# Optimization experiments

Hardware: AMD Instinct MI355X
Metric: run time of the kernel (lower is better)

Reference implementation:

```python
import jax, jax.numpy as jnp
import numpy as np

N, E, G = 10000, 40000, 128          # nodes, edges, graphs
NF, EF, H, NH, GD, L = 92, 50, 64, 10, 108, 5  # feat dims, hidden, heads, global dim, layers
EPS = 1e-5

def _lrelu(v):
    return jax.nn.leaky_relu(v, 0.2)

def setup_inputs() -> dict:
    key = jax.random.key(0)
    ks = jax.random.split(key, 24)
    def rn(k, shp, s=0.05):
        return jax.random.normal(k, shp, jnp.float32) * s
    return {
        "x": jax.random.normal(ks[0], (N, NF), jnp.float32),
        "edge_index": jax.random.randint(ks[1], (2, E), 0, N, dtype=jnp.int32),
        "edge_attr": jax.random.normal(ks[2], (E, EF), jnp.float32),
        "batch_idx": jnp.sort(jax.random.randint(ks[3], (N,), 0, G, dtype=jnp.int32)),
        "global_features": jax.random.normal(ks[4], (G, GD), jnp.float32),
        "node_W": rn(ks[5], (NF, H)), "node_b": jnp.zeros((H,), jnp.float32),
        "edge_W": rn(ks[6], (EF, H)), "edge_b": jnp.zeros((H,), jnp.float32),
        "conv_W": rn(ks[7], (L, 2 * H, NH * H)),
        "conv_att": rn(ks[8], (L, NH, 2 * H)),
        "conv_b": jnp.zeros((L, H), jnp.float32),
        "conv_gamma": jnp.ones((L, NH), jnp.float32),
        "conv_beta": jnp.zeros((L, NH), jnp.float32),
        "ga_W1": rn(ks[9], (H + GD, H)), "ga_b1": jnp.zeros((H,), jnp.float32),
        "ga_W2": rn(ks[10], (H, 1)), "ga_b2": jnp.zeros((1,), jnp.float32),
        "out_W1": rn(ks[11], (H, H)), "out_b1": jnp.zeros((H,), jnp.float32),
        "out_W2": rn(ks[12], (H, 1)), "out_b2": jnp.zeros((1,), jnp.float32),
    }

def reference(x, edge_index, edge_attr, batch_idx, global_features,
              node_W, node_b, edge_W, edge_b,
              conv_W, conv_att, conv_b, conv_gamma, conv_beta,
              ga_W1, ga_b1, ga_W2, ga_b2, out_W1, out_b1, out_W2, out_b2):
    row, col = edge_index[0], edge_index[1]
    # embeddings
    h = _lrelu(x @ node_W + node_b)            # [N, H]
    ea = _lrelu(edge_attr @ edge_W + edge_b)   # [E, H]
    initial = h
    inv_std = 1.0 / jnp.sqrt(1.0 + EPS)        # DiffGroupNorm eval: running mean=0, var=1
    for i in range(L):
        xi = jnp.concatenate([h[row], ea], axis=-1)               # [E, 2H]
        xj = jnp.concatenate([h[col], ea], axis=-1)
        hi = _lrelu(xi @ conv_W[i]).reshape(E, NH, H)             # [E, NH, H]
        hj = _lrelu(xj @ conv_W[i]).reshape(E, NH, H)
        alpha = jnp.sum(jnp.concatenate([hi, hj], -1) * conv_att[i][None], -1)  # [E, NH]
        alpha = _lrelu(alpha)
        alpha = alpha * inv_std * conv_gamma[i] + conv_beta[i]
        alpha = jax.nn.softmax(alpha, axis=1)                     # softmax over heads
        msg = (hj * alpha[..., None]).reshape(E, NH * H)
        agg = jax.ops.segment_sum(msg, row, num_segments=N).reshape(N, NH, H)
        h_new = agg.mean(axis=1) + conv_b[i]
        h = h + h_new if i > 0 else h_new
    h = h + initial
    # global attention: softmax over nodes within each graph
    g = global_features[batch_idx]                                 # [N, GD]
    s = _lrelu(jnp.concatenate([h, g], -1) @ ga_W1 + ga_b1)
    score = (s @ ga_W2 + ga_b2)[:, 0]                              # [N]
    smax = jax.ops.segment_max(score, batch_idx, num_segments=G)
    ex = jnp.exp(score - smax[batch_idx])
    denom = jax.ops.segment_sum(ex, batch_idx, num_segments=G)
    w = (ex / denom[batch_idx])[:, None]
    h = h * w
    pooled = jax.ops.segment_sum(h, batch_idx, num_segments=G)     # [G, H]
    out = jax.nn.relu(pooled @ out_W1 + out_b1) @ out_W2 + out_b2
    return out[:, 0]
```

## Files before the change

### kernel.cpp

```cpp
#include <hip/hip_runtime.h>

#define LRELU(v) ((v) > 0.f ? (v) : 0.2f * (v))

template <int CTRL, int RMASK>
__device__ __forceinline__ float dpp_add(float v) {
  int moved = __builtin_amdgcn_update_dpp(0, __builtin_bit_cast(int, v), CTRL,
                                          RMASK, 0xf, true);
  return v + __builtin_bit_cast(float, moved);
}
__device__ __forceinline__ float wave_sum(float v) {
  v = dpp_add<0x111, 0xf>(v);
  v = dpp_add<0x112, 0xf>(v);
  v = dpp_add<0x114, 0xf>(v);
  v = dpp_add<0x118, 0xf>(v);
  v = dpp_add<0x142, 0xa>(v);
  v = dpp_add<0x143, 0xc>(v);
  return __builtin_bit_cast(
      float, __builtin_amdgcn_readlane(__builtin_bit_cast(int, v), 63));
}

__global__ __launch_bounds__(256) void embed2_kernel(
    const float* __restrict__ x, const float* __restrict__ nW,
    const float* __restrict__ nb, float* __restrict__ h0, int N_,
    const float* __restrict__ eattr, const float* __restrict__ eW,
    const float* __restrict__ eb, float* __restrict__ ea, int E_,
    int nodeBlocks) {
  const int lane = threadIdx.x & 63;
  const float *X, *W, *b;
  float* out;
  int M, K, r;
  if ((int)blockIdx.x < nodeBlocks) {
    r = blockIdx.x * 4 + (threadIdx.x >> 6);
    X = x; W = nW; b = nb; out = h0; M = N_; K = 92;
  } else {
    r = (blockIdx.x - nodeBlocks) * 4 + (threadIdx.x >> 6);
    X = eattr; W = eW; b = eb; out = ea; M = E_; K = 50;
  }
  r = __builtin_amdgcn_readfirstlane(r);
  if (r >= M) return;
  float acc = b[lane];
  const float* Xr = X + (size_t)r * K;
  const float* Wl = W + lane;
  for (int k = 0; k < K; ++k) acc = fmaf(Xr[k], Wl[(size_t)k * 64], acc);
  acc = LRELU(acc);
  out[(size_t)r * 64 + lane] = acc;
}

__global__ __launch_bounds__(256, 4) void update_gemm_kernel(
    const float* __restrict__ A0, float* __restrict__ h,
    float* __restrict__ agg, const float* __restrict__ bvec,
    const float* __restrict__ W, float* __restrict__ P, int M, int mode) {
  const int lane = threadIdx.x & 63;
  const int wv =
      __builtin_amdgcn_readfirstlane(blockIdx.x * 4 + (threadIdx.x >> 6));
  const int r0 = wv * 4;
  if (r0 >= M) return;
  float hv[4];
  if (mode < 0) {
#pragma unroll
    for (int r = 0; r < 4; ++r) hv[r] = A0[(size_t)(r0 + r) * 64 + lane];
  } else {
    float bl = bvec[lane];
#pragma unroll
    for (int r = 0; r < 4; ++r) {
      size_t idx = (size_t)(r0 + r) * 64 + lane;
      float v = fmaf(agg[idx], 0.1f, bl);
      if (mode >= 1) v += h[idx];
      agg[idx] = 0.f;
      h[idx] = v;
      hv[r] = v;
    }
  }
  float acc[4][10];
#pragma unroll
  for (int r = 0; r < 4; ++r)
#pragma unroll
    for (int q = 0; q < 10; ++q) acc[r][q] = 0.f;
  const float* Wl = W + lane;
  float wa[10], wb[10];
#pragma unroll
  for (int q = 0; q < 10; ++q) wa[q] = Wl[q * 64];
#pragma unroll 1
  for (int k = 0; k < 64; k += 2) {
#pragma unroll
    for (int q = 0; q < 10; ++q) wb[q] = Wl[(k + 1) * 640 + q * 64];
#pragma unroll
    for (int r = 0; r < 4; ++r) {
      float a = __shfl(hv[r], k);
#pragma unroll
      for (int q = 0; q < 10; ++q) acc[r][q] = fmaf(a, wa[q], acc[r][q]);
    }
    if (k + 2 < 64) {
#pragma unroll
      for (int q = 0; q < 10; ++q) wa[q] = Wl[(k + 2) * 640 + q * 64];
    }
#pragma unroll
    for (int r = 0; r < 4; ++r) {
      float a = __shfl(hv[r], k + 1);
#pragma unroll
      for (int q = 0; q < 10; ++q) acc[r][q] = fmaf(a, wb[q], acc[r][q]);
    }
  }
#pragma unroll
  for (int r = 0; r < 4; ++r) {
    float* Crow = P + (size_t)(r0 + r) * 640;
#pragma unroll
    for (int q = 0; q < 10; ++q) Crow[q * 64 + lane] = acc[r][q];
  }
}

__global__ __launch_bounds__(256, 4) void edge_fused_kernel(
    const float* __restrict__ P, const float* __restrict__ ea,
    const float* __restrict__ Wbot,
    const int* __restrict__ row, const int* __restrict__ col,
    const float* __restrict__ att, const float* __restrict__ gamma,
    const float* __restrict__ beta, float* __restrict__ agg, int E_) {
  const int lane = threadIdx.x & 63;
  const int wv =
      __builtin_amdgcn_readfirstlane(blockIdx.x * 4 + (threadIdx.x >> 6));
  const int e0 = wv * 8;
  if (e0 >= E_) return;

  int eix[8], ris[8], cis[8];
#pragma unroll
  for (int r = 0; r < 8; ++r) {
    int e = (e0 + r < E_) ? (e0 + r) : (E_ - 1);
    eix[r] = e;
    ris[r] = row[e];
    cis[r] = col[e];
  }

  const float inv_std = 0.9999950000374997f;
  float m[8];
  float mx[8], ss[8];
#pragma unroll
  for (int r = 0; r < 8; ++r) {
    m[r] = 0.f;
    mx[r] = -1e30f;
    ss[r] = 0.f;
  }

#pragma unroll 1
  for (int c = 0; c < 2; ++c) {
    float qacc[8][5];
#pragma unroll
    for (int r = 0; r < 8; ++r)
#pragma unroll
      for (int q = 0; q < 5; ++q) qacc[r][q] = 0.f;
    const float* Wl = Wbot + c * 320 + lane;
    float wa[5], wb[5];
#pragma unroll
    for (int q = 0; q < 5; ++q) wa[q] = Wl[q * 64];
#pragma unroll 1
    for (int k = 0; k < 64; k += 2) {
#pragma unroll
      for (int q = 0; q < 5; ++q) wb[q] = Wl[(k + 1) * 640 + q * 64];
#pragma unroll
      for (int r = 0; r < 8; ++r) {
        float a = ea[(size_t)eix[r] * 64 + k];
#pragma unroll
        for (int q = 0; q < 5; ++q) qacc[r][q] = fmaf(a, wa[q], qacc[r][q]);
      }
      if (k + 2 < 64) {
#pragma unroll
        for (int q = 0; q < 5; ++q) wa[q] = Wl[(k + 2) * 640 + q * 64];
      }
#pragma unroll
      for (int r = 0; r < 8; ++r) {
        float a = ea[(size_t)eix[r] * 64 + k + 1];
#pragma unroll
        for (int q = 0; q < 5; ++q) qacc[r][q] = fmaf(a, wb[q], qacc[r][q]);
      }
    }

    float at_i[5], at_j[5];
    float gm[5], bt[5];
#pragma unroll
    for (int q = 0; q < 5; ++q) {
      at_i[q] = att[(c * 5 + q) * 128 + lane];
      at_j[q] = att[(c * 5 + q) * 128 + 64 + lane];
      gm[q] = gamma[c * 5 + q];
      bt[q] = beta[c * 5 + q];
    }

    float prb[5], pcb[5];
    {
      const float* Pr = P + (size_t)ris[0] * 640 + c * 320 + lane;
      const float* Pc = P + (size_t)cis[0] * 640 + c * 320 + lane;
#pragma unroll
      for (int q = 0; q < 5; ++q) {
        prb[q] = Pr[q * 64];
        pcb[q] = Pc[q * 64];
      }
    }

#pragma unroll
    for (int r = 0; r < 8; ++r) {
      if (e0 + r >= E_) break;
      float pr[5], pc[5];
#pragma unroll
      for (int q = 0; q < 5; ++q) {
        pr[q] = prb[q];
        pc[q] = pcb[q];
      }
      if (r + 1 < 8) {
        const float* Pr = P + (size_t)ris[r + 1] * 640 + c * 320 + lane;
        const float* Pc = P + (size_t)cis[r + 1] * 640 + c * 320 + lane;
#pragma unroll
        for (int q = 0; q < 5; ++q) {
          prb[q] = Pr[q * 64];
          pcb[q] = Pc[q * 64];
        }
      }
      float hj[5], sv[5];
#pragma unroll
      for (int q = 0; q < 5; ++q) {
        float qc = qacc[r][q];
        float hi = pr[q] + qc;
        float hjv = pc[q] + qc;
        hi = LRELU(hi);
        hjv = LRELU(hjv);
        hj[q] = hjv;
        float part = fmaf(hi, at_i[q], hjv * at_j[q]);
        sv[q] = wave_sum(part);
      }
      float mxc = -1e30f;
#pragma unroll
      for (int q = 0; q < 5; ++q) {
        float a = sv[q];
        a = LRELU(a);
        a = fmaf(a * inv_std, gm[q], bt[q]);
        sv[q] = a;
        mxc = fmaxf(mxc, a);
      }
      float nm = fmaxf(mx[r], mxc);
      float scale = __expf(mx[r] - nm);
      float sum5 = 0.f;
#pragma unroll
      for (int q = 0; q < 5; ++q) {
        float ex = __expf(sv[q] - nm);
        sv[q] = ex;
        sum5 += ex;
      }
      ss[r] = fmaf(ss[r], scale, sum5);
      float add = 0.f;
#pragma unroll
      for (int q = 0; q < 5; ++q) add = fmaf(sv[q], hj[q], add);
      m[r] = fmaf(m[r], scale, add);
      mx[r] = nm;
    }
  }

#pragma unroll
  for (int r = 0; r < 8; ++r) {
    if (e0 + r >= E_) break;
    atomicAdd(agg + (size_t)ris[r] * 64 + lane, m[r] / ss[r]);
  }
}

__global__ __launch_bounds__(256) void finalize_kernel(
    float* __restrict__ h, float* __restrict__ agg, const float* __restrict__ b,
    const float* __restrict__ h0, int total) {
  int idx = blockIdx.x * 256 + threadIdx.x;
  if (idx >= total) return;
  int f = idx & 63;
  float v = fmaf(agg[idx], 0.1f, b[f]);
  agg[idx] = 0.f;
  h[idx] = v + h[idx] + h0[idx];
}

__global__ __launch_bounds__(256) void score_kernel(
    const float* __restrict__ h, const int* __restrict__ batch,
    const float* __restrict__ gf, const float* __restrict__ W1,
    const float* __restrict__ b1, const float* __restrict__ W2,
    const float* __restrict__ b2, float* __restrict__ score, int N_) {
  const int lane = threadIdx.x & 63;
  const int n =
      __builtin_amdgcn_readfirstlane(blockIdx.x * 4 + (threadIdx.x >> 6));
  if (n >= N_) return;
  float acc = b1[lane];
  const float* hn = h + (size_t)n * 64;
  const float* W1l = W1 + lane;
#pragma unroll 8
  for (int k = 0; k < 64; ++k) acc = fmaf(hn[k], W1l[k * 64], acc);
  const int bn = batch[n];
  const float* g = gf + (size_t)bn * 108;
#pragma unroll 4
  for (int k = 0; k < 108; ++k) acc = fmaf(g[k], W1l[(64 + k) * 64], acc);
  acc = LRELU(acc);
  float v = wave_sum(acc * W2[lane]);
  if (lane == 0) score[n] = v + b2[0];
}

__global__ void bounds_kernel(const int* __restrict__ batch,
                              int* __restrict__ start, int N_, int G_) {
  int n = blockIdx.x * blockDim.x + threadIdx.x;
  if (n >= N_) return;
  int b = batch[n];
  int bp = (n == 0) ? -1 : batch[n - 1];
  for (int g = bp + 1; g <= b; ++g) start[g] = n;
  if (n == N_ - 1)
    for (int g = b + 1; g <= G_; ++g) start[g] = N_;
}

__global__ __launch_bounds__(256) void pool_out_kernel(
    const float* __restrict__ h, const float* __restrict__ score,
    const int* __restrict__ start, const float* __restrict__ W1,
    const float* __restrict__ b1, const float* __restrict__ W2,
    const float* __restrict__ b2, float* __restrict__ out) {
  int g = blockIdx.x;
  int s0 = start[g], s1 = start[g + 1];
  int tid = threadIdx.x;
  __shared__ float red[256];
  __shared__ float pool[64];
  __shared__ float sh_smax, sh_denom;
  float lm = -1e30f;
  for (int n = s0 + tid; n < s1; n += 256) lm = fmaxf(lm, score[n]);
  red[tid] = lm;
  __syncthreads();
  for (int off = 128; off; off >>= 1) {
    if (tid < off) red[tid] = fmaxf(red[tid], red[tid + off]);
    __syncthreads();
  }
  if (tid == 0) sh_smax = red[0];
  __syncthreads();
  float smax = sh_smax;
  __syncthreads();
  float ls = 0.f;
  for (int n = s0 + tid; n < s1; n += 256) ls += __expf(score[n] - smax);
  red[tid] = ls;
  __syncthreads();
  for (int off = 128; off; off >>= 1) {
    if (tid < off) red[tid] += red[tid + off];
    __syncthreads();
  }
  if (tid == 0) sh_denom = red[0];
  __syncthreads();
  float denom = sh_denom;
  float invd = denom > 0.f ? 1.0f / denom : 0.f;
  __syncthreads();
  int f = tid & 63, sub = tid >> 6;
  float acc = 0.f;
  for (int n = s0 + sub; n < s1; n += 4)
    acc = fmaf(__expf(score[n] - smax), h[(size_t)n * 64 + f], acc);
  red[tid] = acc;
  __syncthreads();
  if (tid < 64)
    pool[tid] =
        (red[tid] + red[tid + 64] + red[tid + 128] + red[tid + 192]) * invd;
  __syncthreads();
  if (tid < 64) {
    float a = b1[tid];
#pragma unroll 8
    for (int k = 0; k < 64; ++k) a = fmaf(pool[k], W1[k * 64 + tid], a);
    a = fmaxf(a, 0.f);
    red[tid] = a * W2[tid];
  }
  __syncthreads();
  if (tid == 0) {
    float s = 0.f;
    for (int k = 0; k < 64; ++k) s += red[k];
    out[g] = s + b2[0];
  }
}

extern "C" void kernel_launch(void* const* d_in, const int* in_sizes, int n_in,
                              void* d_out, int out_size, void* d_ws,
                              size_t ws_size, hipStream_t stream) {
  const float* x          = (const float*)d_in[0];
  const int*   edge_index = (const int*)d_in[1];
  const float* edge_attr  = (const float*)d_in[2];
  const int*   batch_idx  = (const int*)d_in[3];
  const float* gf         = (const float*)d_in[4];
  const float* node_W     = (const float*)d_in[5];
  const float* node_b     = (const float*)d_in[6];
  const float* edge_W     = (const float*)d_in[7];
  const float* edge_b     = (const float*)d_in[8];
  const float* conv_W     = (const float*)d_in[9];
  const float* conv_att   = (const float*)d_in[10];
  const float* conv_b     = (const float*)d_in[11];
  const float* conv_gamma = (const float*)d_in[12];
  const float* conv_beta  = (const float*)d_in[13];
  const float* ga_W1      = (const float*)d_in[14];
  const float* ga_b1      = (const float*)d_in[15];
  const float* ga_W2      = (const float*)d_in[16];
  const float* ga_b2      = (const float*)d_in[17];
  const float* out_W1     = (const float*)d_in[18];
  const float* out_b1     = (const float*)d_in[19];
  const float* out_W2     = (const float*)d_in[20];
  const float* out_b2     = (const float*)d_in[21];
  float* out = (float*)d_out;

  const int N = in_sizes[3];
  const int E = in_sizes[2] / 50;
  const int G = in_sizes[4] / 108;
  const int L = 5;

  float* ws = (float*)d_ws;
  float* h    = ws;  ws += (size_t)N * 64;
  float* h0   = ws;  ws += (size_t)N * 64;
  float* ea   = ws;  ws += (size_t)E * 64;
  float* P    = ws;  ws += (size_t)N * 640;
  float* agg  = ws;  ws += (size_t)N * 64;
  float* scr  = ws;  ws += N;
  int* gstart = (int*)ws;

  const int* row = edge_index;
  const int* col = edge_index + E;

  int nodeBlocks = (N + 3) / 4;
  int edgeBlocks = (E + 3) / 4;
  embed2_kernel<<<nodeBlocks + edgeBlocks, 256, 0, stream>>>(
      x, node_W, node_b, h0, N, edge_attr, edge_W, edge_b, ea, E, nodeBlocks);
  (void)hipMemsetAsync(agg, 0, (size_t)N * 64 * sizeof(float), stream);

  for (int i = 0; i < L; ++i) {
    const float* Wi = conv_W + (size_t)i * 128 * 640;
    if (i == 0) {
      update_gemm_kernel<<<(N / 4 + 3) / 4, 256, 0, stream>>>(
          h0, h, agg, nullptr, Wi, P, N, -1);
    } else {
      update_gemm_kernel<<<(N / 4 + 3) / 4, 256, 0, stream>>>(
          nullptr, h, agg, conv_b + (i - 1) * 64, Wi, P, N,
          (i - 1) == 0 ? 0 : 1);
    }
    int waves = (E + 7) / 8;
    edge_fused_kernel<<<(waves + 3) / 4, 256, 0, stream>>>(
        P, ea, Wi + 64 * 640, row, col, conv_att + (size_t)i * 1280,
        conv_gamma + i * 10, conv_beta + i * 10, agg, E);
  }
  finalize_kernel<<<(N * 64 + 255) / 256, 256, 0, stream>>>(
      h, agg, conv_b + (L - 1) * 64, h0, N * 64);

  score_kernel<<<(N + 3) / 4, 256, 0, stream>>>(h, batch_idx, gf, ga_W1, ga_b1,
                                                ga_W2, ga_b2, scr, N);
  bounds_kernel<<<(N + 255) / 256, 256, 0, stream>>>(batch_idx, gstart, N, G);
  pool_out_kernel<<<G, 256, 0, stream>>>(h, scr, gstart, out_W1, out_b1, out_W2,
                                         out_b2, out);
}
```

Before: 792.1 us.

## Split edge kernel head halves across wave pairs with LDS softmax exchange

Each group of 8 edges is now handled by two waves, each computing 5 of the 10 heads, instead of one wave looping serially over both head halves. The two waves exchange attention logits and partial messages through shared memory, joined by two block-wide barriers, before one wave issues the atomic adds. This doubles the wave count and halves the serial work per wave to expose more parallelism. In exchange it adds LDS traffic and barriers, and keeps hj[8][5] live in registers, which raises register pressure.

Result: faster. 750.9 us (-5.2%).

```diff
diff --git a/kernel.cpp b/kernel.cpp
--- a/kernel.cpp
+++ b/kernel.cpp
@@ -115,39 +115,33 @@
     const int* __restrict__ row, const int* __restrict__ col,
     const float* __restrict__ att, const float* __restrict__ gamma,
     const float* __restrict__ beta, float* __restrict__ agg, int E_) {
-  const int lane = threadIdx.x & 63;
-  const int wv =
-      __builtin_amdgcn_readfirstlane(blockIdx.x * 4 + (threadIdx.x >> 6));
-  const int e0 = wv * 8;
-  if (e0 >= E_) return;
+  __shared__ float lg[2][8][10];
+  __shared__ float mb[2][8][64];
+  const int tid = threadIdx.x;
+  const int lane = tid & 63;
+  const int wid = tid >> 6;
+  const int pairi = wid >> 1, half = wid & 1;
+  const int pidx = __builtin_amdgcn_readfirstlane(blockIdx.x * 2 + pairi);
+  const int e0 = pidx * 8;
+  const bool active = e0 < E_;
+  const int e0c = active ? e0 : 0;
 
   int eix[8], ris[8], cis[8];
 #pragma unroll
   for (int r = 0; r < 8; ++r) {
-    int e = (e0 + r < E_) ? (e0 + r) : (E_ - 1);
+    int e = (e0c + r < E_) ? (e0c + r) : (E_ - 1);
     eix[r] = e;
     ris[r] = row[e];
     cis[r] = col[e];
   }
 
-  const float inv_std = 0.9999950000374997f;
-  float m[8];
-  float mx[8], ss[8];
-#pragma unroll
-  for (int r = 0; r < 8; ++r) {
-    m[r] = 0.f;
-    mx[r] = -1e30f;
-    ss[r] = 0.f;
-  }
-
-#pragma unroll 1
-  for (int c = 0; c < 2; ++c) {
-    float qacc[8][5];
-#pragma unroll
-    for (int r = 0; r < 8; ++r)
-#pragma unroll
-      for (int q = 0; q < 5; ++q) qacc[r][q] = 0.f;
-    const float* Wl = Wbot + c * 320 + lane;
+  float qacc[8][5];
+#pragma unroll
+  for (int r = 0; r < 8; ++r)
+#pragma unroll
+    for (int q = 0; q < 5; ++q) qacc[r][q] = 0.f;
+  {
+    const float* Wl = Wbot + half * 320 + lane;
     float wa[5], wb[5];
 #pragma unroll
     for (int q = 0; q < 5; ++q) wa[q] = Wl[q * 64];
@@ -172,89 +166,102 @@
         for (int q = 0; q < 5; ++q) qacc[r][q] = fmaf(a, wb[q], qacc[r][q]);
       }
     }
-
-    float at_i[5], at_j[5];
-    float gm[5], bt[5];
+  }
+
+  const float inv_std = 0.9999950000374997f;
+  float at_i[5], at_j[5];
+  float gm[5], bt[5];
+#pragma unroll
+  for (int q = 0; q < 5; ++q) {
+    at_i[q] = att[(half * 5 + q) * 128 + lane];
+    at_j[q] = att[(half * 5 + q) * 128 + 64 + lane];
+    gm[q] = gamma[half * 5 + q];
+    bt[q] = beta[half * 5 + q];
+  }
+
+  float prb[5], pcb[5];
+  {
+    const float* Pr = P + (size_t)ris[0] * 640 + half * 320 + lane;
+    const float* Pc = P + (size_t)cis[0] * 640 + half * 320 + lane;
 #pragma unroll
     for (int q = 0; q < 5; ++q) {
-      at_i[q] = att[(c * 5 + q) * 128 + lane];
-      at_j[q] = att[(c * 5 + q) * 128 + 64 + lane];
-      gm[q] = gamma[c * 5 + q];
-      bt[q] = beta[c * 5 + q];
-    }
-
-    float prb[5], pcb[5];
-    {
-      const float* Pr = P + (size_t)ris[0] * 640 + c * 320 + lane;
-      const float* Pc = P + (size_t)cis[0] * 640 + c * 320 + lane;
+      prb[q] = Pr[q * 64];
+      pcb[q] = Pc[q * 64];
+    }
+  }
+
+  float hj[8][5];
+#pragma unroll
+  for (int r = 0; r < 8; ++r) {
+    float pr[5], pc[5];
+#pragma unroll
+    for (int q = 0; q < 5; ++q) {
+      pr[q] = prb[q];
+      pc[q] = pcb[q];
+    }
+    if (r + 1 < 8) {
+      const float* Pr = P + (size_t)ris[r + 1] * 640 + half * 320 + lane;
+      const float* Pc = P + (size_t)cis[r + 1] * 640 + half * 320 + lane;
 #pragma unroll
       for (int q = 0; q < 5; ++q) {
         prb[q] = Pr[q * 64];
         pcb[q] = Pc[q * 64];
       }
     }
-
+    float lq[5];
+#pragma unroll
+    for (int q = 0; q < 5; ++q) {
+      float qc = qacc[r][q];
+      float hi = pr[q] + qc;
+      float hjv = pc[q] + qc;
+      hi = LRELU(hi);
+      hjv = LRELU(hjv);
+      hj[r][q] = hjv;
+      float part = fmaf(hi, at_i[q], hjv * at_j[q]);
+      float s = wave_sum(part);
+      float a = LRELU(s);
+      lq[q] = fmaf(a * inv_std, gm[q], bt[q]);
+    }
+    if (lane == 0) {
+#pragma unroll
+      for (int q = 0; q < 5; ++q) lg[pairi][r][half * 5 + q] = lq[q];
+    }
+  }
+  __syncthreads();
+
+  float m[8];
+#pragma unroll
+  for (int r = 0; r < 8; ++r) {
+    float v[10];
+#pragma unroll
+    for (int j = 0; j < 10; ++j) v[j] = lg[pairi][r][j];
+    float mx = -1e30f;
+#pragma unroll
+    for (int j = 0; j < 10; ++j) mx = fmaxf(mx, v[j]);
+    float ssum = 0.f;
+    float ex5[5];
+#pragma unroll
+    for (int j = 0; j < 10; ++j) {
+      float ex = __expf(v[j] - mx);
+      ssum += ex;
+      int q = j - half * 5;
+      if (q >= 0 && q < 5) ex5[q] = ex;
+    }
+    float inv = 1.0f / ssum;
+    float acc = 0.f;
+#pragma unroll
+    for (int q = 0; q < 5; ++q) acc = fmaf(ex5[q] * inv, hj[r][q], acc);
+    m[r] = acc;
+    if (half == 1) mb[pairi][r][lane] = acc;
+  }
+  __syncthreads();
+
+  if (active && half == 0) {
 #pragma unroll
     for (int r = 0; r < 8; ++r) {
       if (e0 + r >= E_) break;
-      float pr[5], pc[5];
-#pragma unroll
-      for (int q = 0; q < 5; ++q) {
-        pr[q] = prb[q];
-        pc[q] = pcb[q];
-      }
-      if (r + 1 < 8) {
-        const float* Pr = P + (size_t)ris[r + 1] * 640 + c * 320 + lane;
-        const float* Pc = P + (size_t)cis[r + 1] * 640 + c * 320 + lane;
-#pragma unroll
-        for (int q = 0; q < 5; ++q) {
-          prb[q] = Pr[q * 64];
-          pcb[q] = Pc[q * 64];
-        }
-      }
-      float hj[5], sv[5];
-#pragma unroll
-      for (int q = 0; q < 5; ++q) {
-        float qc = qacc[r][q];
-        float hi = pr[q] + qc;
-        float hjv = pc[q] + qc;
-        hi = LRELU(hi);
-        hjv = LRELU(hjv);
-        hj[q] = hjv;
-        float part = fmaf(hi, at_i[q], hjv * at_j[q]);
-        sv[q] = wave_sum(part);
-      }
-      float mxc = -1e30f;
-#pragma unroll
-      for (int q = 0; q < 5; ++q) {
-        float a = sv[q];
-        a = LRELU(a);
-        a = fmaf(a * inv_std, gm[q], bt[q]);
-        sv[q] = a;
-        mxc = fmaxf(mxc, a);
-      }
-      float nm = fmaxf(mx[r], mxc);
-      float scale = __expf(mx[r] - nm);
-      float sum5 = 0.f;
-#pragma unroll
-      for (int q = 0; q < 5; ++q) {
-        float ex = __expf(sv[q] - nm);
-        sv[q] = ex;
-        sum5 += ex;
-      }
-      ss[r] = fmaf(ss[r], scale, sum5);
-      float add = 0.f;
-#pragma unroll
-      for (int q = 0; q < 5; ++q) add = fmaf(sv[q], hj[q], add);
-      m[r] = fmaf(m[r], scale, add);
-      mx[r] = nm;
-    }
-  }
-
-#pragma unroll
-  for (int r = 0; r < 8; ++r) {
-    if (e0 + r >= E_) break;
-    atomicAdd(agg + (size_t)ris[r] * 64 + lane, m[r] / ss[r]);
+      atomicAdd(agg + (size_t)ris[r] * 64 + lane, m[r] + mb[pairi][r][lane]);
+    }
   }
 }
 
@@ -424,8 +431,8 @@
           nullptr, h, agg, conv_b + (i - 1) * 64, Wi, P, N,
           (i - 1) == 0 ? 0 : 1);
     }
-    int waves = (E + 7) / 8;
-    edge_fused_kernel<<<(waves + 3) / 4, 256, 0, stream>>>(
+    int pairs = (E + 7) / 8;
+    edge_fused_kernel<<<(pairs + 1) / 2, 256, 0, stream>>>(
         P, ea, Wi + 64 * 640, row, col, conv_att + (size_t)i * 1280,
         conv_gamma + i * 10, conv_beta + i * 10, agg, E);
   }
```
